# Optimization experiments

Hardware: AMD Instinct MI355X
Metric: run time of the kernel (lower is better)

Reference implementation:

```python
import jax, jax.numpy as jnp
from jax import lax
import numpy as np

# Reconstructed utils constants
PSZ = 24     # patch size
KS = 3       # kernel size of generated conv kernels
FILTERS = 9  # channels / number of generated filters
STRIDE = 8   # conv stride inside KGL


def setup_inputs() -> dict:
    key = jax.random.key(0)
    k1, k2, k3 = jax.random.split(key, 3)
    B, H, W = 8, 768, 768
    x = jax.random.normal(k1, (B, H, W, FILTERS), dtype=jnp.float32)
    conv_w = jax.random.normal(k2, (KS, KS, FILTERS, 9), dtype=jnp.float32) * 0.05  # HWIO
    conv_b = jnp.zeros((9,), dtype=jnp.float32)
    dense_w = jax.random.normal(k3, (FILTERS, FILTERS * FILTERS), dtype=jnp.float32) * 0.05
    dense_b = jnp.zeros((FILTERS * FILTERS,), dtype=jnp.float32)
    return {"x": x, "conv_w": conv_w, "conv_b": conv_b, "dense_w": dense_w, "dense_b": dense_b}


def _clip_by_norm(t, axes, clip_norm=1.0):
    # tf.clip_by_norm: t * clip_norm / max(||t||_2_over_axes, clip_norm)
    l2 = jnp.sqrt(jnp.sum(t * t, axis=axes, keepdims=True))
    return t * (clip_norm / jnp.maximum(l2, clip_norm))


def reference(x, conv_w, conv_b, dense_w, dense_b):
    B, H, W, C = x.shape
    p1, p2 = H // PSZ, W // PSZ
    N = p1 * p2
    # tf.image.extract_patches layout: [B, p1, p2, PSZ*PSZ*C] with patch flattened row-major (row, col, chan)
    patches = x.reshape(B, p1, PSZ, p2, PSZ, C).transpose(0, 1, 3, 2, 4, 5)  # [B,p1,p2,PSZ,PSZ,C]
    # RAW reshape to (N, B, PSZ, PSZ, C) exactly as the TF code does (buffer reinterpretation)
    patches = patches.reshape(N, B, PSZ, PSZ, C)
    flat = patches.reshape(N * B, PSZ, PSZ, C)

    # --- W_G1: per-patch conv kernel generation ---
    conv_out = lax.conv_general_dilated(
        flat, conv_w, window_strides=(STRIDE, STRIDE), padding="SAME",
        dimension_numbers=("NHWC", "HWIO", "NHWC")) + conv_b  # [N*B, 3, 3, 9]
    wg1 = conv_out.reshape(N * B, KS, KS, FILTERS, 1)
    wg1 = _clip_by_norm(wg1, axes=(1, 2))                      # norm over (KS, KS) dims
    wg1 = wg1.reshape(N, B, KS, KS, FILTERS, 1)

    # --- W_G2: per-patch 1x1 mixing kernel via GAP + Dense ---
    gap = flat.mean(axis=(1, 2))                               # [N*B, C]
    d = gap @ dense_w + dense_b                                # [N*B, FILTERS^2]
    wg2 = d.reshape(N * B, 1, 1, FILTERS, FILTERS)
    wg2 = _clip_by_norm(wg2, axes=(1, 2, 3))
    wg2 = wg2.reshape(N, B, 1, 1, FILTERS, FILTERS)
    return wg1, wg2
```

## Files before the change

kernel.cpp:

```cpp
#include <hip/hip_runtime.h>


#define PSZ 24
#define NCH 9
#define HW 768
#define PATCH_ELEMS (PSZ*PSZ*NCH)
#define PATCH_V4 1296
#define NPIX (PSZ*PSZ)
#define ROWF (PSZ*NCH)
#define ROWV4 54
#define XROWF (HW*NCH)
#define OUT2_OFF 663552

__device__ inline void async_load16(const void* g, void* l) {
    __builtin_amdgcn_global_load_lds(
        (const __attribute__((address_space(1))) void*)g,
        (__attribute__((address_space(3))) void*)l, 16, 0, 0);
}

__global__ __launch_bounds__(256) void kgl_kernel(
    const float* __restrict__ x,
    const float* __restrict__ conv_w,
    const float* __restrict__ conv_b,
    const float* __restrict__ dense_w,
    const float* __restrict__ dense_b,
    float* __restrict__ out)
{
    __shared__ __align__(16) float patch[PATCH_ELEMS];
    __shared__ __align__(16) float cwA[732];
    __shared__ __align__(16) float cwB[732];
    __shared__ __align__(16) float colA[ROWF];
    __shared__ __align__(16) float colB[ROWF];
    __shared__ float gapA[NCH];
    __shared__ float gapB[NCH];
    __shared__ float co_s[81];
    __shared__ float d_s[81];

    const int j   = blockIdx.x;
    const int b   = j >> 10;
    const int rem = j & 1023;
    const int pi  = rem >> 5;
    const int pj  = rem & 31;
    const int tid = threadIdx.x;

    const size_t base = ((size_t)(b*HW + pi*PSZ) * HW + (size_t)pj*PSZ) * NCH;

    float conv_acc = 0.f;

    if (tid < 128) {
        float* cw = (tid < 64) ? cwA : cwB;
        const int lane = tid & 63;
        #pragma unroll
        for (int i = 0; i < 3; ++i) {
            int e = lane + i*64;
            if (e < 182)
                reinterpret_cast<float4*>(cw)[e] =
                    reinterpret_cast<const float4*>(conv_w)[e];
        }
        if (lane == 0) cw[728] = conv_w[728];

        if (tid < 81) {
            const int oy = tid / 27;
            const int ox = (tid / 9) % 3;
            const int oc = tid % 9;
            float acc = conv_b[oc];
            #pragma unroll
            for (int ky = 0; ky < 3; ++ky) {
                const float* gp = x + base + (size_t)(oy*8+ky)*XROWF + (size_t)(ox*8)*NCH;
                const float4* gp4 = reinterpret_cast<const float4*>(gp);
                float pv[27];
                #pragma unroll
                for (int q = 0; q < 6; ++q) {
                    float4 v = gp4[q];
                    pv[q*4+0] = v.x; pv[q*4+1] = v.y; pv[q*4+2] = v.z; pv[q*4+3] = v.w;
                }
                pv[24] = gp[24]; pv[25] = gp[25]; pv[26] = gp[26];
                #pragma unroll
                for (int kx = 0; kx < 3; ++kx) {
                    #pragma unroll
                    for (int ic = 0; ic < 9; ++ic)
                        acc += pv[kx*9+ic] * cw[(ky*3+kx)*81 + ic*9 + oc];
                }
            }
            co_s[tid] = acc;
            conv_acc = acc;
        }
    } else {
        const float* gbase = x + base;
        #pragma unroll
        for (int it = 0; it < 11; ++it) {
            int e4 = (tid - 128) + it*128;
            if (e4 < PATCH_V4) {
                int r = e4 / ROWV4;
                int t = e4 - r*ROWV4;
                async_load16(gbase + (size_t)r*XROWF + t*4, &patch[e4*4]);
            }
        }
    }
    __syncthreads();

    if (tid < 81) {
        const int oc = tid % 9;
        float n2 = 0.f;
        #pragma unroll
        for (int s = 0; s < 9; ++s) {
            float v = co_s[s*9 + oc];
            n2 += v*v;
        }
        float sc = 1.0f / fmaxf(sqrtf(n2), 1.0f);
        out[(size_t)j*81 + tid] = conv_acc * sc;
    } else if (tid >= 128) {
        const int w  = (tid >= 192) ? 1 : 0;
        const int k  = tid & 63;
        float* col   = w ? colB : colA;
        const int r0 = w ? 12 : 0;
        if (k < ROWV4) {
            const float4* pv = reinterpret_cast<const float4*>(patch);
            float4 acc = pv[r0*ROWV4 + k];
            #pragma unroll
            for (int r = 1; r < 12; ++r) {
                float4 v = pv[(r0+r)*ROWV4 + k];
                acc.x += v.x; acc.y += v.y; acc.z += v.z; acc.w += v.w;
            }
            reinterpret_cast<float4*>(col)[k] = acc;
        }
        if (k < NCH) {
            float s = 0.f;
            #pragma unroll
            for (int i = 0; i < 24; ++i) s += col[k + NCH*i];
            if (w) gapB[k] = s; else gapA[k] = s;
        }
    }
    __syncthreads();

    if (tid < 81) {
        float d = dense_b[tid];
        #pragma unroll
        for (int c = 0; c < NCH; ++c)
            d += (gapA[c] + gapB[c]) * (1.0f/(float)NPIX) * dense_w[c*81 + tid];
        d_s[tid] = d;
    }
    __syncthreads();

    if (tid < 81) {
        const int bc = tid % 9;
        float n2 = 0.f;
        #pragma unroll
        for (int a = 0; a < 9; ++a) {
            float v = d_s[a*9 + bc];
            n2 += v*v;
        }
        float sc = 1.0f / fmaxf(sqrtf(n2), 1.0f);
        out[OUT2_OFF + (size_t)j*81 + tid] = d_s[tid] * sc;
    }
}

extern "C" void kernel_launch(void* const* d_in, const int* in_sizes, int n_in,
                              void* d_out, int out_size, void* d_ws, size_t ws_size,
                              hipStream_t stream) {
    const float* x       = (const float*)d_in[0];
    const float* conv_w  = (const float*)d_in[1];
    const float* conv_b  = (const float*)d_in[2];
    const float* dense_w = (const float*)d_in[3];
    const float* dense_b = (const float*)d_in[4];
    float* out = (float*)d_out;

    kgl_kernel<<<8192, 256, 0, stream>>>(x, conv_w, conv_b, dense_w, dense_b, out);
}
```

Measured before the change: 241.5 us.

## Reduce patch rows directly from global memory instead of staging in LDS

The global-average-pool warps now read their twelve patch rows straight from global memory into float4 registers and accumulate them. This replaces the async global-to-LDS copy of the whole 24x24x9 patch followed by an LDS reduction. Dropping the roughly 20 KB shared patch buffer and one barrier phase frees LDS for more resident blocks per CU and shortens the dependency chain. The conv path also now uses a seventh float4 load instead of three scalar loads, reading one float past the 27 it needs. The risk is that the global loads are issued less asynchronously than the LDS DMA path.

```diff
diff --git a/kernel.cpp b/kernel.cpp
--- a/kernel.cpp
+++ b/kernel.cpp
@@ -4,19 +4,11 @@
 #define PSZ 24
 #define NCH 9
 #define HW 768
-#define PATCH_ELEMS (PSZ*PSZ*NCH)
-#define PATCH_V4 1296
 #define NPIX (PSZ*PSZ)
 #define ROWF (PSZ*NCH)
 #define ROWV4 54
 #define XROWF (HW*NCH)
 #define OUT2_OFF 663552
-
-__device__ inline void async_load16(const void* g, void* l) {
-    __builtin_amdgcn_global_load_lds(
-        (const __attribute__((address_space(1))) void*)g,
-        (__attribute__((address_space(3))) void*)l, 16, 0, 0);
-}
 
 __global__ __launch_bounds__(256) void kgl_kernel(
     const float* __restrict__ x,
@@ -26,7 +18,6 @@
     const float* __restrict__ dense_b,
     float* __restrict__ out)
 {
-    __shared__ __align__(16) float patch[PATCH_ELEMS];
     __shared__ __align__(16) float cwA[732];
     __shared__ __align__(16) float cwB[732];
     __shared__ __align__(16) float colA[ROWF];
@@ -44,6 +35,7 @@
     const int tid = threadIdx.x;
 
     const size_t base = ((size_t)(b*HW + pi*PSZ) * HW + (size_t)pj*PSZ) * NCH;
+    const float* gbase = x + base;
 
     float conv_acc = 0.f;
 
@@ -66,15 +58,14 @@
             float acc = conv_b[oc];
             #pragma unroll
             for (int ky = 0; ky < 3; ++ky) {
-                const float* gp = x + base + (size_t)(oy*8+ky)*XROWF + (size_t)(ox*8)*NCH;
+                const float* gp = gbase + (size_t)(oy*8+ky)*XROWF + (size_t)(ox*8)*NCH;
                 const float4* gp4 = reinterpret_cast<const float4*>(gp);
-                float pv[27];
+                float pv[28];
                 #pragma unroll
-                for (int q = 0; q < 6; ++q) {
+                for (int q = 0; q < 7; ++q) {
                     float4 v = gp4[q];
                     pv[q*4+0] = v.x; pv[q*4+1] = v.y; pv[q*4+2] = v.z; pv[q*4+3] = v.w;
                 }
-                pv[24] = gp[24]; pv[25] = gp[25]; pv[26] = gp[26];
                 #pragma unroll
                 for (int kx = 0; kx < 3; ++kx) {
                     #pragma unroll
@@ -86,15 +77,25 @@
             conv_acc = acc;
         }
     } else {
-        const float* gbase = x + base;
-        #pragma unroll
-        for (int it = 0; it < 11; ++it) {
-            int e4 = (tid - 128) + it*128;
-            if (e4 < PATCH_V4) {
-                int r = e4 / ROWV4;
-                int t = e4 - r*ROWV4;
-                async_load16(gbase + (size_t)r*XROWF + t*4, &patch[e4*4]);
+        const int w  = (tid >= 192) ? 1 : 0;
+        const int k  = tid & 63;
+        const int r0 = w ? 12 : 0;
+        if (k < ROWV4) {
+            float4 acc = make_float4(0.f, 0.f, 0.f, 0.f);
+            #pragma unroll
+            for (int r = 0; r < 12; ++r) {
+                float4 v = *reinterpret_cast<const float4*>(
+                    gbase + (size_t)(r0 + r)*XROWF + (size_t)k*4);
+                acc.x += v.x; acc.y += v.y; acc.z += v.z; acc.w += v.w;
             }
+            reinterpret_cast<float4*>(w ? colB : colA)[k] = acc;
+        }
+        if (k < NCH) {
+            const float* col = w ? colB : colA;
+            float s = 0.f;
+            #pragma unroll
+            for (int i = 0; i < 24; ++i) s += col[k + NCH*i];
+            if (w) gapB[k] = s; else gapA[k] = s;
         }
     }
     __syncthreads();
@@ -109,31 +110,7 @@
         }
         float sc = 1.0f / fmaxf(sqrtf(n2), 1.0f);
         out[(size_t)j*81 + tid] = conv_acc * sc;
-    } else if (tid >= 128) {
-        const int w  = (tid >= 192) ? 1 : 0;
-        const int k  = tid & 63;
-        float* col   = w ? colB : colA;
-        const int r0 = w ? 12 : 0;
-        if (k < ROWV4) {
-            const float4* pv = reinterpret_cast<const float4*>(patch);
-            float4 acc = pv[r0*ROWV4 + k];
-            #pragma unroll
-            for (int r = 1; r < 12; ++r) {
-                float4 v = pv[(r0+r)*ROWV4 + k];
-                acc.x += v.x; acc.y += v.y; acc.z += v.z; acc.w += v.w;
-            }
-            reinterpret_cast<float4*>(col)[k] = acc;
-        }
-        if (k < NCH) {
-            float s = 0.f;
-            #pragma unroll
-            for (int i = 0; i < 24; ++i) s += col[k + NCH*i];
-            if (w) gapB[k] = s; else gapA[k] = s;
-        }
-    }
-    __syncthreads();
 
-    if (tid < 81) {
         float d = dense_b[tid];
         #pragma unroll
         for (int c = 0; c < NCH; ++c)
```

Result: no change. 238.9 us, median of 2 (-1.1%).
